# Performance work log

Hardware: AMD Instinct MI355X
Metric: run time of the kernel (lower is better)

Reference implementation:

```python
import jax, jax.numpy as jnp
import numpy as np
from jax import lax

D_MODEL = 64
D_STATE = 128
D_INNER = 128  # d_model * expand_factor; must equal D_STATE for the original code to broadcast
BATCH = 4
SEQ = 1024
LN_EPS = 1e-5


def setup_inputs() -> dict:
    key = jax.random.key(0)
    ks = jax.random.split(key, 12)
    s = 0.05
    return {
        "x": jax.random.normal(ks[0], (BATCH, SEQ, D_MODEL), jnp.float32),
        "W_in": jax.random.normal(ks[1], (2 * D_INNER, D_MODEL), jnp.float32) * s,
        "W_delta": jax.random.normal(ks[2], (D_INNER, D_MODEL), jnp.float32) * s,
        "b_delta": jax.random.normal(ks[3], (D_INNER,), jnp.float32) * s,
        "W_B": jax.random.normal(ks[4], (D_STATE, D_MODEL), jnp.float32) * s,
        "b_B": jax.random.normal(ks[5], (D_STATE,), jnp.float32) * s,
        "W_C": jax.random.normal(ks[6], (D_STATE, D_MODEL), jnp.float32) * s,
        "b_C": jax.random.normal(ks[7], (D_STATE,), jnp.float32) * s,
        "A": jax.random.normal(ks[8], (D_INNER, D_STATE), jnp.float32) * 0.01,
        "W_out": jax.random.normal(ks[9], (D_MODEL, D_INNER), jnp.float32) * s,
        "ln_w": jnp.ones((D_MODEL,), jnp.float32),
        "ln_b": jnp.zeros((D_MODEL,), jnp.float32),
    }


def _layer_norm(x, w, b):
    mu = x.mean(-1, keepdims=True)
    var = ((x - mu) ** 2).mean(-1, keepdims=True)
    return (x - mu) * lax.rsqrt(var + LN_EPS) * w + b


def reference(x, W_in, W_delta, b_delta, W_B, b_B, W_C, b_C, A, W_out, ln_w, ln_b):
    # projections
    xp = jnp.einsum('bld,ed->ble', x, W_in)            # (B, L, 2*d_inner)
    x_ssm, gate = xp[..., :D_INNER], xp[..., D_INNER:]
    delta = jax.nn.softplus(jnp.einsum('bld,id->bli', x, W_delta) + b_delta)  # (B, L, d_inner)
    Bm = jnp.einsum('bld,sd->bls', x, W_B) + b_B        # (B, L, d_state)
    Cm = jnp.einsum('bld,sd->bls', x, W_C) + b_C        # (B, L, d_state)

    # A_discrete.mean(dim=1): mean over d_inner of exp(delta * A)
    Abar = jnp.exp(delta[..., :, None] * A).mean(axis=2)  # (B, L, d_state)
    x_pool = x_ssm.mean(axis=-1)                          # (B, L) mean over d_inner
    Bx = Bm * x_pool[..., None]                           # (B, L, d_state)

    def step(h, inp):
        a_t, bx_t, c_t = inp                              # each (B, d_state)
        h = a_t * h + bx_t
        y = (c_t * h).sum(axis=-1)                        # (B,)
        return h, y

    h0 = jnp.zeros((x.shape[0], D_STATE), x.dtype)
    _, ys = lax.scan(step, h0,
                     (jnp.swapaxes(Abar, 0, 1), jnp.swapaxes(Bx, 0, 1), jnp.swapaxes(Cm, 0, 1)))
    y = jnp.swapaxes(ys, 0, 1)[..., None]                 # (B, L, 1) -> broadcast over d_inner

    y = y * jax.nn.silu(gate)                             # (B, L, d_inner)
    out = jnp.einsum('bli,di->bld', y, W_out)             # (B, L, d_model)
    return _layer_norm(out + x, ln_w, ln_b)
```

## Files before the change

### kernel.cpp

```cpp
#include <hip/hip_runtime.h>
#include <math.h>

#define NB   4
#define SL   1024
#define NTOK (NB*SL)
#define DM   64
#define DI   128
#define DSt  128
#define SEGLEN 16
#define NSEG (SL/SEGLEN)

#define OFF_GATE   0
#define OFF_DELTA  (OFF_GATE  + NTOK*DI)
#define OFF_BM     (OFF_DELTA + NTOK*DI)
#define OFF_CM     (OFF_BM    + NTOK*DSt)
#define OFF_XPOOL  (OFF_CM    + NTOK*DSt)
#define OFF_ABAR   (OFF_XPOOL + NTOK)
#define OFF_HEND   (OFF_DELTA)
#define OFF_P      (OFF_DELTA + NB*NSEG*DSt)

#define PROJ_TOK 32
#define PROJ_TG  (NTOK/PROJ_TOK)

static __device__ __forceinline__ float wave64_sum(float v) {
#pragma unroll
    for (int m = 32; m >= 1; m >>= 1) v += __shfl_xor(v, m, 64);
    return v;
}

__global__ __launch_bounds__(256) void k_proj(
    const float* __restrict__ x, const float* __restrict__ W_in,
    const float* __restrict__ W_delta, const float* __restrict__ b_delta,
    const float* __restrict__ W_B, const float* __restrict__ b_B,
    const float* __restrict__ W_C, const float* __restrict__ b_C,
    float* __restrict__ ws)
{
    __shared__ float  xl[PROJ_TOK*DM];
    __shared__ float4 Wl[DI*16];
    const int tid = threadIdx.x;
    const int l   = tid & 63;
    const int w   = tid >> 6;
    const int cat = blockIdx.x >> 7;
    const int tg  = blockIdx.x & (PROJ_TG-1);
    const int tok0 = tg * PROJ_TOK;

    const float* Wbase; const float* bias; float* dst;
    if      (cat == 0) { Wbase = W_in + DI*DM; bias = nullptr; dst = ws + OFF_GATE;  }
    else if (cat == 1) { Wbase = W_delta;      bias = b_delta; dst = ws + OFF_DELTA; }
    else if (cat == 2) { Wbase = W_B;          bias = b_B;     dst = ws + OFF_BM;    }
    else               { Wbase = W_C;          bias = b_C;     dst = ws + OFF_CM;    }

    {
        const float4* xg = (const float4*)(x + tok0*DM);
        float4* xl4 = (float4*)xl;
        xl4[tid]       = xg[tid];
        xl4[tid + 256] = xg[tid + 256];
        const float4* Wg = (const float4*)Wbase;
#pragma unroll
        for (int j = 0; j < 8; ++j) {
            const int f = tid + j*256;
            const int row = f >> 4, k = f & 15;
            Wl[row*16 + (k ^ (row & 15))] = Wg[f];
        }
    }
    __syncthreads();

    float4 w0[16], w1[16];
#pragma unroll
    for (int k = 0; k < 16; ++k) {
        w0[k] = Wl[l*16      + (k ^ (l & 15))];
        w1[k] = Wl[(l+64)*16 + (k ^ (l & 15))];
    }
    float bias0 = 0.f, bias1 = 0.f;
    if (bias) { bias0 = bias[l]; bias1 = bias[l+64]; }

#pragma unroll 2
    for (int it = 0; it < PROJ_TOK/4; ++it) {
        const int tl = it*4 + w;
        float a0=0.f,a1=0.f,a2=0.f,a3=0.f, c0=0.f,c1=0.f,c2=0.f,c3=0.f;
#pragma unroll
        for (int k = 0; k < 16; ++k) {
            const float4 xv = *(const float4*)(xl + tl*DM + 4*k);
            a0 = fmaf(w0[k].x, xv.x, a0);
            a1 = fmaf(w0[k].y, xv.y, a1);
            a2 = fmaf(w0[k].z, xv.z, a2);
            a3 = fmaf(w0[k].w, xv.w, a3);
            c0 = fmaf(w1[k].x, xv.x, c0);
            c1 = fmaf(w1[k].y, xv.y, c1);
            c2 = fmaf(w1[k].z, xv.z, c2);
            c3 = fmaf(w1[k].w, xv.w, c3);
        }
        float ra = (a0+a1) + (a2+a3) + bias0;
        float rb = (c0+c1) + (c2+c3) + bias1;
        if (cat == 1) {
            ra = fmaxf(ra, 0.f) + log1pf(__expf(-fabsf(ra)));
            rb = fmaxf(rb, 0.f) + log1pf(__expf(-fabsf(rb)));
        }
        const int tok = tok0 + tl;
        dst[tok*128 + l]      = ra;
        dst[tok*128 + 64 + l] = rb;
    }

    if (cat == 0) {
        float wp = 0.f;
#pragma unroll 8
        for (int i = 0; i < DI; ++i) wp += W_in[i*DM + l];
        wp *= (1.0f/DI);
#pragma unroll
        for (int it = 0; it < PROJ_TOK/4; ++it) {
            const int tl = it*4 + w;
            float v = xl[tl*DM + l] * wp;
            v = wave64_sum(v);
            if (l == 0) ws[OFF_XPOOL + tok0 + tl] = v;
        }
    }
}

__global__ __launch_bounds__(256, 2) void k_abar(const float* __restrict__ A,
                                                 float* __restrict__ ws)
{
    const int tid  = threadIdx.x;
    const int s    = tid & 127;
    const int half = tid >> 7;
    float areg[DI];
#pragma unroll
    for (int i = 0; i < DI; ++i) areg[i] = A[i*DSt + s];

    const float* delta = ws + OFF_DELTA;
    float*       Abar  = ws + OFF_ABAR;
    const int base = blockIdx.x * 8 + half * 4;
#pragma unroll
    for (int p = 0; p < 4; ++p) {
        const int tok = base + p;
        const float* dv = delta + tok*DI;
        float a0 = 0.f, a1 = 0.f, a2 = 0.f, a3 = 0.f;
#pragma unroll
        for (int i4 = 0; i4 < DI/4; ++i4) {
            const float4 d4 = *(const float4*)(dv + 4*i4);
            a0 += __expf(d4.x * areg[4*i4    ]);
            a1 += __expf(d4.y * areg[4*i4 + 1]);
            a2 += __expf(d4.z * areg[4*i4 + 2]);
            a3 += __expf(d4.w * areg[4*i4 + 3]);
        }
        Abar[tok*DSt + s] = ((a0+a1) + (a2+a3)) * (1.0f/DI);
    }
}

__global__ __launch_bounds__(128) void k_scan1(float* __restrict__ ws)
{
    const int s   = threadIdx.x;
    const int b   = blockIdx.x >> 6;
    const int seg = blockIdx.x & 63;
    const float* Abar  = ws + OFF_ABAR;
    const float* Bm    = ws + OFF_BM;
    const float* xpool = ws + OFF_XPOOL;
    float h = 0.f, p = 1.f;
    const int t0 = b*SL + seg*SEGLEN;
#pragma unroll
    for (int t = 0; t < SEGLEN; ++t) {
        const float a  = Abar[(t0 + t)*DSt + s];
        const float bx = Bm[(t0 + t)*DSt + s] * xpool[t0 + t];
        h = fmaf(a, h, bx);
        p *= a;
    }
    ws[OFF_HEND + blockIdx.x*DSt + s] = h;
    ws[OFF_P    + blockIdx.x*DSt + s] = p;
}

__global__ __launch_bounds__(256) void k_scan2_out(
    const float* __restrict__ x, const float* __restrict__ W_out,
    const float* __restrict__ ln_w, const float* __restrict__ ln_b,
    float* __restrict__ ws, float* __restrict__ out)
{
    __shared__ float  prod[2*SEGLEN][132];
    __shared__ float4 Wl[DM*32];
    __shared__ float  vbuf[4][DI];
    __shared__ float  y_lds[2*SEGLEN];

    const int tid   = threadIdx.x;
    const int lane  = tid & 63;
    const int w     = tid >> 6;
    const int shalf = tid & 127;
    const int wp    = tid >> 7;
    const int b     = blockIdx.x >> 5;
    const int sg    = blockIdx.x & 31;
    const int seg   = sg*2 + wp;

    const float4* W4g = (const float4*)W_out;
#pragma unroll
    for (int j = 0; j < 8; ++j) {
        const int f = tid + j*256;
        const int row = f >> 5, c4 = f & 31;
        Wl[row*32 + (c4 ^ (row & 7))] = W4g[f];
    }

    const float* Abar  = ws + OFF_ABAR;
    const float* Bm    = ws + OFF_BM;
    const float* Cm    = ws + OFF_CM;
    const float* xpool = ws + OFF_XPOOL;
    const float* hend  = ws + OFF_HEND;
    const float* P     = ws + OFF_P;

    float h = 0.f;
#pragma unroll 4
    for (int j = 0; j < seg; ++j) {
        const int idx = (b*NSEG + j)*DSt + shalf;
        h = fmaf(P[idx], h, hend[idx]);
    }
    const int t0 = b*SL + seg*SEGLEN;
#pragma unroll
    for (int t = 0; t < SEGLEN; ++t) {
        const float a  = Abar[(t0 + t)*DSt + shalf];
        const float bx = Bm[(t0 + t)*DSt + shalf] * xpool[t0 + t];
        h = fmaf(a, h, bx);
        prod[wp*SEGLEN + t][shalf] = Cm[(t0 + t)*DSt + shalf] * h;
    }
    __syncthreads();

    {
        const int t = shalf >> 3, r = lane & 7;
        const int row = wp*SEGLEN + t;
        float4 acc4 = {0.f,0.f,0.f,0.f};
#pragma unroll
        for (int k4 = 0; k4 < 4; ++k4) {
            const float4 v = *(const float4*)(&prod[row][r*16 + 4*k4]);
            acc4.x += v.x; acc4.y += v.y; acc4.z += v.z; acc4.w += v.w;
        }
        float acc = (acc4.x + acc4.y) + (acc4.z + acc4.w);
#pragma unroll
        for (int m = 1; m <= 4; m <<= 1) acc += __shfl_xor(acc, m, 64);
        if (r == 0) y_lds[row] = acc;
    }
    __syncthreads();

    const float* gate = ws + OFF_GATE;
    const int d = lane;
    const float lw = ln_w[d], lb = ln_b[d];
#pragma unroll 2
    for (int j = 0; j < 8; ++j) {
        const int tloc = w*8 + j;
        const int tok  = b*SL + sg*32 + tloc;
        const float yt = y_lds[tloc];
        const float g0 = gate[tok*DI + d];
        const float g1 = gate[tok*DI + 64 + d];
        vbuf[w][d]      = yt * (g0 / (1.f + __expf(-g0)));
        vbuf[w][64 + d] = yt * (g1 / (1.f + __expf(-g1)));

        float ac0 = 0.f, ac1 = 0.f, ac2 = 0.f, ac3 = 0.f;
#pragma unroll 8
        for (int q = 0; q < 32; ++q) {
            const float4 wv = Wl[d*32 + (q ^ (d & 7))];
            const float4 vv = *(const float4*)(&vbuf[w][q*4]);
            ac0 = fmaf(wv.x, vv.x, ac0);
            ac1 = fmaf(wv.y, vv.y, ac1);
            ac2 = fmaf(wv.z, vv.z, ac2);
            ac3 = fmaf(wv.w, vv.w, ac3);
        }
        const float z  = (ac0+ac1) + (ac2+ac3) + x[tok*DM + d];
        const float s1 = wave64_sum(z);
        const float s2 = wave64_sum(z*z);
        const float mu  = s1 * (1.f/64.f);
        const float var = s2 * (1.f/64.f) - mu*mu;
        out[tok*DM + d] = (z - mu) * rsqrtf(var + 1e-5f) * lw + lb;
    }
}

extern "C" void kernel_launch(void* const* d_in, const int* in_sizes, int n_in,
                              void* d_out, int out_size, void* d_ws, size_t ws_size,
                              hipStream_t stream) {
    const float* x       = (const float*)d_in[0];
    const float* W_in    = (const float*)d_in[1];
    const float* W_delta = (const float*)d_in[2];
    const float* b_delta = (const float*)d_in[3];
    const float* W_B     = (const float*)d_in[4];
    const float* b_B     = (const float*)d_in[5];
    const float* W_C     = (const float*)d_in[6];
    const float* b_C     = (const float*)d_in[7];
    const float* A       = (const float*)d_in[8];
    const float* W_out   = (const float*)d_in[9];
    const float* ln_w    = (const float*)d_in[10];
    const float* ln_b    = (const float*)d_in[11];
    float* out = (float*)d_out;
    float* ws  = (float*)d_ws;

    hipLaunchKernelGGL(k_proj,      dim3(4*PROJ_TG), dim3(256), 0, stream,
                       x, W_in, W_delta, b_delta, W_B, b_B, W_C, b_C, ws);
    hipLaunchKernelGGL(k_abar,      dim3(512),  dim3(256), 0, stream, A, ws);
    hipLaunchKernelGGL(k_scan1,     dim3(256),  dim3(128), 0, stream, ws);
    hipLaunchKernelGGL(k_scan2_out, dim3(128),  dim3(256), 0, stream,
                       x, W_out, ln_w, ln_b, ws, out);
}
```

Measured before the change: 53.26 us.

## Fuse Abar computation with segment scan and use native exp2

Merges the Abar kernel and the first scan pass into one kernel, one block per 16-token segment, so segment end states are computed from LDS-resident Abar without a separate launch or global reload. Exp is replaced by the hardware v_exp_f32 exp2 instruction with A prescaled by log2(e). In the second scan kernel, the Abar/Bm/Cm loads are hoisted ahead of the serial prefix loop so their latency overlaps it. The fused kernel launches only 256 blocks instead of 512, which halves grid parallelism for the exp-heavy part, and hend/P move to their own workspace region.

```diff
diff --git a/kernel.cpp b/kernel.cpp
--- a/kernel.cpp
+++ b/kernel.cpp
@@ -16,8 +16,8 @@
 #define OFF_CM     (OFF_BM    + NTOK*DSt)
 #define OFF_XPOOL  (OFF_CM    + NTOK*DSt)
 #define OFF_ABAR   (OFF_XPOOL + NTOK)
-#define OFF_HEND   (OFF_DELTA)
-#define OFF_P      (OFF_DELTA + NB*NSEG*DSt)
+#define OFF_HEND   (OFF_ABAR  + NTOK*DSt)
+#define OFF_P      (OFF_HEND  + NB*NSEG*DSt)
 
 #define PROJ_TOK 32
 #define PROJ_TG  (NTOK/PROJ_TOK)
@@ -26,6 +26,12 @@
 #pragma unroll
     for (int m = 32; m >= 1; m >>= 1) v += __shfl_xor(v, m, 64);
     return v;
+}
+
+static __device__ __forceinline__ float fast_exp2(float x) {
+    float r;
+    asm("v_exp_f32 %0, %1" : "=v"(r) : "v"(x));
+    return r;
 }
 
 __global__ __launch_bounds__(256) void k_proj(
@@ -116,55 +122,59 @@
     }
 }
 
-__global__ __launch_bounds__(256, 2) void k_abar(const float* __restrict__ A,
-                                                 float* __restrict__ ws)
+__global__ __launch_bounds__(256, 2) void k_abar_scan1(const float* __restrict__ A,
+                                                       float* __restrict__ ws)
 {
+    __shared__ float ab_lds[SEGLEN][DSt];
     const int tid  = threadIdx.x;
     const int s    = tid & 127;
     const int half = tid >> 7;
+    const int b    = blockIdx.x >> 6;
+    const int seg  = blockIdx.x & 63;
+    const int t0   = b*SL + seg*SEGLEN;
+
     float areg[DI];
 #pragma unroll
-    for (int i = 0; i < DI; ++i) areg[i] = A[i*DSt + s];
+    for (int i = 0; i < DI; ++i) areg[i] = A[i*DSt + s] * 1.44269504f;
 
     const float* delta = ws + OFF_DELTA;
     float*       Abar  = ws + OFF_ABAR;
-    const int base = blockIdx.x * 8 + half * 4;
-#pragma unroll
-    for (int p = 0; p < 4; ++p) {
-        const int tok = base + p;
-        const float* dv = delta + tok*DI;
+#pragma unroll 2
+    for (int p = 0; p < 8; ++p) {
+        const int tl = half*8 + p;
+        const float* dv = delta + (t0 + tl)*DI;
         float a0 = 0.f, a1 = 0.f, a2 = 0.f, a3 = 0.f;
 #pragma unroll
         for (int i4 = 0; i4 < DI/4; ++i4) {
             const float4 d4 = *(const float4*)(dv + 4*i4);
-            a0 += __expf(d4.x * areg[4*i4    ]);
-            a1 += __expf(d4.y * areg[4*i4 + 1]);
-            a2 += __expf(d4.z * areg[4*i4 + 2]);
-            a3 += __expf(d4.w * areg[4*i4 + 3]);
-        }
-        Abar[tok*DSt + s] = ((a0+a1) + (a2+a3)) * (1.0f/DI);
-    }
-}
-
-__global__ __launch_bounds__(128) void k_scan1(float* __restrict__ ws)
-{
-    const int s   = threadIdx.x;
-    const int b   = blockIdx.x >> 6;
-    const int seg = blockIdx.x & 63;
-    const float* Abar  = ws + OFF_ABAR;
-    const float* Bm    = ws + OFF_BM;
-    const float* xpool = ws + OFF_XPOOL;
-    float h = 0.f, p = 1.f;
-    const int t0 = b*SL + seg*SEGLEN;
-#pragma unroll
-    for (int t = 0; t < SEGLEN; ++t) {
-        const float a  = Abar[(t0 + t)*DSt + s];
-        const float bx = Bm[(t0 + t)*DSt + s] * xpool[t0 + t];
-        h = fmaf(a, h, bx);
-        p *= a;
-    }
-    ws[OFF_HEND + blockIdx.x*DSt + s] = h;
-    ws[OFF_P    + blockIdx.x*DSt + s] = p;
+            a0 += fast_exp2(d4.x * areg[4*i4    ]);
+            a1 += fast_exp2(d4.y * areg[4*i4 + 1]);
+            a2 += fast_exp2(d4.z * areg[4*i4 + 2]);
+            a3 += fast_exp2(d4.w * areg[4*i4 + 3]);
+        }
+        const float ab = ((a0+a1) + (a2+a3)) * (1.0f/DI);
+        ab_lds[tl][s] = ab;
+        Abar[(t0 + tl)*DSt + s] = ab;
+    }
+    __syncthreads();
+
+    if (tid < 128) {
+        const float* Bm    = ws + OFF_BM;
+        const float* xpool = ws + OFF_XPOOL;
+        float bx[SEGLEN];
+#pragma unroll
+        for (int t = 0; t < SEGLEN; ++t)
+            bx[t] = Bm[(t0 + t)*DSt + s] * xpool[t0 + t];
+        float h = 0.f, pr = 1.f;
+#pragma unroll
+        for (int t = 0; t < SEGLEN; ++t) {
+            const float a = ab_lds[t][s];
+            h = fmaf(a, h, bx[t]);
+            pr *= a;
+        }
+        ws[OFF_HEND + blockIdx.x*DSt + s] = h;
+        ws[OFF_P    + blockIdx.x*DSt + s] = pr;
+    }
 }
 
 __global__ __launch_bounds__(256) void k_scan2_out(
@@ -201,19 +211,26 @@
     const float* hend  = ws + OFF_HEND;
     const float* P     = ws + OFF_P;
 
+    const int t0 = b*SL + seg*SEGLEN;
+
+    float aA[SEGLEN], aB[SEGLEN], aC[SEGLEN];
+#pragma unroll
+    for (int t = 0; t < SEGLEN; ++t) {
+        aA[t] = Abar[(t0 + t)*DSt + shalf];
+        aB[t] = Bm[(t0 + t)*DSt + shalf] * xpool[t0 + t];
+        aC[t] = Cm[(t0 + t)*DSt + shalf];
+    }
+
     float h = 0.f;
-#pragma unroll 4
+#pragma unroll 8
     for (int j = 0; j < seg; ++j) {
         const int idx = (b*NSEG + j)*DSt + shalf;
         h = fmaf(P[idx], h, hend[idx]);
     }
-    const int t0 = b*SL + seg*SEGLEN;
 #pragma unroll
     for (int t = 0; t < SEGLEN; ++t) {
-        const float a  = Abar[(t0 + t)*DSt + shalf];
-        const float bx = Bm[(t0 + t)*DSt + shalf] * xpool[t0 + t];
-        h = fmaf(a, h, bx);
-        prod[wp*SEGLEN + t][shalf] = Cm[(t0 + t)*DSt + shalf] * h;
+        h = fmaf(aA[t], h, aB[t]);
+        prod[wp*SEGLEN + t][shalf] = aC[t] * h;
     }
     __syncthreads();
 
@@ -283,10 +300,9 @@
     float* out = (float*)d_out;
     float* ws  = (float*)d_ws;
 
-    hipLaunchKernelGGL(k_proj,      dim3(4*PROJ_TG), dim3(256), 0, stream,
+    hipLaunchKernelGGL(k_proj,       dim3(4*PROJ_TG), dim3(256), 0, stream,
                        x, W_in, W_delta, b_delta, W_B, b_B, W_C, b_C, ws);
-    hipLaunchKernelGGL(k_abar,      dim3(512),  dim3(256), 0, stream, A, ws);
-    hipLaunchKernelGGL(k_scan1,     dim3(256),  dim3(128), 0, stream, ws);
-    hipLaunchKernelGGL(k_scan2_out, dim3(128),  dim3(256), 0, stream,
+    hipLaunchKernelGGL(k_abar_scan1, dim3(NB*NSEG),   dim3(256), 0, stream, A, ws);
+    hipLaunchKernelGGL(k_scan2_out,  dim3(128),       dim3(256), 0, stream,
                        x, W_out, ln_w, ln_b, ws, out);
 }
```

Result: slower. 76.01 us (+42.7%).
